# Performance work log

Measured on AMD Instinct MI355X. Metric: run time of the kernel, lower is better.

## Reference

```python
import jax, jax.numpy as jnp
import numpy as np

B, C, W, H = 4, 256, 64, 64
D = C // 8  # reduced query/key channels


def setup_inputs() -> dict:
    key = jax.random.key(0)
    k1, k2, k3, k4, k5 = jax.random.split(key, 5)
    return {
        "x": jax.random.normal(k1, (B, C, W, H), dtype=jnp.float32),
        "q_weight": jax.random.normal(k2, (D, C), dtype=jnp.float32) * 0.05,
        "k_weight": jax.random.normal(k3, (D, C), dtype=jnp.float32) * 0.05,
        "v_weight": jax.random.normal(k4, (C, C), dtype=jnp.float32) * 0.05,
        "gamma": jax.random.normal(k5, (1,), dtype=jnp.float32),
    }


def reference(x, q_weight, k_weight, v_weight, gamma):
    b, c, w, h = x.shape
    n = w * h
    xf = x.reshape(b, c, n)                       # (B, C, N)
    # 1x1 convs == channel matmuls
    q = jnp.einsum('dc,bcn->bdn', q_weight, xf)   # (B, D, N)
    k = jnp.einsum('dc,bcn->bdn', k_weight, xf)   # (B, D, N)
    v = jnp.einsum('oc,bcn->bon', v_weight, xf)   # (B, C, N)
    # energy[b, i, j] = <q[:, i], k[:, j]>  (unscaled, single head)
    energy = jnp.einsum('bdi,bdj->bij', q, k)     # (B, N, N)
    attn = jax.nn.softmax(energy, axis=-1)        # softmax over keys j
    # out[b, c, i] = sum_j v[b, c, j] * attn[b, i, j]
    out = jnp.einsum('bcj,bij->bci', v, attn)     # (B, C, N)
    out = out.reshape(b, c, w, h)
    return gamma[0] * out + x
```

## Files before the change

### kernel.cpp

```cpp
#include <hip/hip_runtime.h>
#include <math.h>

#define Bb 4
#define Cc 256
#define Nn 4096
#define Dd 32
#define CH 128
#define XST 264

typedef __attribute__((ext_vector_type(8))) short bf16x8;
typedef __attribute__((ext_vector_type(4))) float f32x4;

__device__ __forceinline__ unsigned short f2bf(float x) {
    union { float f; unsigned u; } c; c.f = x;
    unsigned r = c.u + 0x7fffu + ((c.u >> 16) & 1u);
    return (unsigned short)(r >> 16);
}
__device__ __forceinline__ unsigned pk2(float a, float b) {
    return (unsigned)f2bf(a) | ((unsigned)f2bf(b) << 16);
}
__device__ __forceinline__ void load_lds16(const void* g, void* l) {
    __builtin_amdgcn_global_load_lds(
        (const __attribute__((address_space(1))) void*)g,
        (__attribute__((address_space(3))) void*)l, 16, 0, 0);
}
__device__ __forceinline__ float fexp2(float x) {
#if __has_builtin(__builtin_amdgcn_exp2f)
    return __builtin_amdgcn_exp2f(x);
#else
    return __exp2f(x);
#endif
}
template <int CTRL>
__device__ __forceinline__ float dppf(float v) {
    int iv = __builtin_bit_cast(int, v);
    return __builtin_bit_cast(float,
        __builtin_amdgcn_update_dpp(iv, iv, CTRL, 0xF, 0xF, false));
}
__device__ __forceinline__ float rowsum16(float v) {
    v += dppf<0xB1>(v);
    v += dppf<0x4E>(v);
    v += dppf<0x141>(v);
    v += dppf<0x140>(v);
    return v;
}

__global__ __launch_bounds__(256) void pack_w(
    const float* __restrict__ qw, const float* __restrict__ kw,
    const float* __restrict__ vw, short* __restrict__ wpk) {
    const int g = blockIdx.x * 256 + threadIdx.x;
    const int qd = g & 3, m = (g >> 2) & 15, kc = (g >> 6) & 7, ot = g >> 9;
    const int o = 16 * ot + m;
    const float* src;
    float scale = 1.0f;
    if (o < 32)      { src = qw + (size_t)o * Cc; scale = 1.44269504088896f; }
    else if (o < 64) { src = kw + (size_t)(o - 32) * Cc; }
    else             { src = vw + (size_t)(o - 64) * Cc; }
    const float* s8 = src + 32 * kc + 8 * qd;
    uint4 u;
    u.x = pk2(s8[0] * scale, s8[1] * scale);
    u.y = pk2(s8[2] * scale, s8[3] * scale);
    u.z = pk2(s8[4] * scale, s8[5] * scale);
    u.w = pk2(s8[6] * scale, s8[7] * scale);
    *(uint4*)(wpk + (size_t)g * 8) = u;
}

__global__ __launch_bounds__(256) void proj(
    const float* __restrict__ x, const short* __restrict__ wpk,
    short* __restrict__ q_t, short* __restrict__ k_t, short* __restrict__ v_b) {
    __shared__ alignas(16) short xs[32 * XST];
    const int b = blockIdx.z;
    const int n0 = blockIdx.x * 32;
    const int tid = threadIdx.x;
    const int w = tid >> 6;
    const int lane = tid & 63, qd = lane >> 4, m = lane & 15;

    {
        const int n = tid & 31, cg = tid >> 5;
        const float* xp = x + ((size_t)b * Cc + 32 * cg) * Nn + n0 + n;
        float xv[32];
#pragma unroll
        for (int i = 0; i < 32; ++i) xv[i] = xp[(size_t)i * Nn];
        short* row = xs + n * XST + 32 * cg;
#pragma unroll
        for (int u4 = 0; u4 < 4; ++u4)
            *(uint4*)(row + 8 * u4) = make_uint4(
                pk2(xv[8*u4+0], xv[8*u4+1]), pk2(xv[8*u4+2], xv[8*u4+3]),
                pk2(xv[8*u4+4], xv[8*u4+5]), pk2(xv[8*u4+6], xv[8*u4+7]));
    }
    __syncthreads();

    const int fslot = m * 4 + qd;
    f32x4 acc[5][2];
#pragma unroll
    for (int i = 0; i < 5; ++i)
#pragma unroll
        for (int nt = 0; nt < 2; ++nt) acc[i][nt] = (f32x4){0.f, 0.f, 0.f, 0.f};

    bf16x8 afc[5], afn[5];
#pragma unroll
    for (int i = 0; i < 5; ++i)
        afc[i] = *(const bf16x8*)(wpk + ((size_t)((4*i + w) * 8 + 0) * 64 + fslot) * 8);

    for (int kc = 0; kc < 8; ++kc) {
        if (kc < 7) {
#pragma unroll
            for (int i = 0; i < 5; ++i)
                afn[i] = *(const bf16x8*)(
                    wpk + ((size_t)((4*i + w) * 8 + kc + 1) * 64 + fslot) * 8);
        }
        const bf16x8 b0 = *(const bf16x8*)&xs[(     m) * XST + 32 * kc + 8 * qd];
        const bf16x8 b1 = *(const bf16x8*)&xs[(16 + m) * XST + 32 * kc + 8 * qd];
#pragma unroll
        for (int i = 0; i < 5; ++i)
            acc[i][0] = __builtin_amdgcn_mfma_f32_16x16x32_bf16(afc[i], b0, acc[i][0], 0, 0, 0);
#pragma unroll
        for (int i = 0; i < 5; ++i)
            acc[i][1] = __builtin_amdgcn_mfma_f32_16x16x32_bf16(afc[i], b1, acc[i][1], 0, 0, 0);
#pragma unroll
        for (int i = 0; i < 5; ++i) afc[i] = afn[i];
    }

#pragma unroll
    for (int i = 0; i < 5; ++i) {
        const int ot = 4 * i + w;
        if (ot < 4) {
            short* dst = (ot < 2 ? q_t : k_t) + (size_t)b * Nn * Dd;
            const int dbase = (ot & 1) * 16 + 4 * qd;
#pragma unroll
            for (int nt = 0; nt < 2; ++nt) {
                const f32x4 a = acc[i][nt];
                *(uint2*)(dst + (size_t)(n0 + 16 * nt + m) * Dd + dbase) =
                    make_uint2(pk2(a[0], a[1]), pk2(a[2], a[3]));
            }
        } else {
            const int cbase = (ot - 4) * 16 + 4 * qd;
            const int gbase = n0 & ~63;
            const int off2 = (n0 & 32) ? 2 : 0;
#pragma unroll
            for (int rr = 0; rr < 4; ++rr) {
                const unsigned pv = pk2(acc[i][0][rr], acc[i][1][rr]);
                *(unsigned*)(v_b + ((size_t)b * Cc + cbase + rr) * Nn +
                             gbase + 4 * m + off2) = pv;
            }
        }
    }
}

__global__ __launch_bounds__(256) void attn(
    const float* __restrict__ x, const short* __restrict__ q_t,
    const short* __restrict__ k_t, const short* __restrict__ v_b,
    const float* __restrict__ gamma, float* __restrict__ out) {
    __shared__ alignas(16) char pool[54528];
    short* q_s = (short*)(pool);
    char*  kv0 = pool + 4096;
    char*  kv1 = pool + 24576;
    short* p_s = (short*)(pool + 45056);
    float* l_s = (float*)(pool + 54272);
    float* o_t = (float*)(pool + 4096);

    const int b = blockIdx.z, cg = blockIdx.y;
    const int i0 = blockIdx.x * 64;
    const int tid = threadIdx.x;
    const int w = tid >> 6, lane = tid & 63;
    const int qd = lane >> 4, m = lane & 15;

    const short* ktb = k_t + (size_t)b * Nn * Dd;
    const short* vtb = v_b + ((size_t)(b * Cc) + cg * CH) * Nn;

    load_lds16(q_t + ((size_t)b * Nn + i0) * Dd + tid * 8, q_s + tid * 8);
    {
        load_lds16(ktb + tid * 8, kv0 + tid * 16);
        short* vls = (short*)(kv0 + 4096);
#pragma unroll
        for (int p = 0; p < 4; ++p) {
            const int cl = 32 * p + (tid >> 3);
            const int j8 = (tid & 7) ^ (cl & 7);
            load_lds16(vtb + (size_t)cl * Nn + j8 * 8, vls + 2048 * p + tid * 8);
        }
    }
    __syncthreads();

    const bf16x8 af = *(const bf16x8*)(q_s + (16 * w + m) * Dd + 8 * qd);

    f32x4 oacc[4][2];
#pragma unroll
    for (int mt = 0; mt < 4; ++mt)
#pragma unroll
        for (int nt = 0; nt < 2; ++nt) oacc[mt][nt] = (f32x4){0.f, 0.f, 0.f, 0.f};
    float l_i[4] = {0.f, 0.f, 0.f, 0.f};

    int cur = 0;
    for (int jt = 0; jt < Nn / 64; ++jt) {
        const char* kvc = cur ? kv1 : kv0;
        const short* k_s = (const short*)kvc;
        const short* v_s = (const short*)(kvc + 4096);

        if (jt) __syncthreads();

        f32x4 sf[4];
#pragma unroll
        for (int nt = 0; nt < 4; ++nt) {
            const bf16x8 bfr = *(const bf16x8*)(k_s + (16 * nt + m) * Dd + 8 * qd);
            sf[nt] = __builtin_amdgcn_mfma_f32_16x16x32_bf16(
                af, bfr, (f32x4){0.f, 0.f, 0.f, 0.f}, 0, 0, 0);
        }

#pragma unroll
        for (int rr = 0; rr < 4; ++rr) {
            float p0 = fexp2(sf[0][rr]);
            float p1 = fexp2(sf[1][rr]);
            float p2 = fexp2(sf[2][rr]);
            float p3 = fexp2(sf[3][rr]);
            l_i[rr] += (p0 + p1) + (p2 + p3);
            *(uint2*)&p_s[(16 * w + 4 * qd + rr) * 72 + 4 * m] =
                make_uint2(pk2(p0, p1), pk2(p2, p3));
        }
        __syncthreads();

        if (jt + 1 < Nn / 64) {
            char* kvn = cur ? kv0 : kv1;
            const int j0n = (jt + 1) * 64;
            load_lds16(ktb + (size_t)j0n * Dd + tid * 8, kvn + tid * 16);
            short* vls = (short*)(kvn + 4096);
#pragma unroll
            for (int p = 0; p < 4; ++p) {
                const int cl = 32 * p + (tid >> 3);
                const int j8 = (tid & 7) ^ (cl & 7);
                load_lds16(vtb + (size_t)cl * Nn + j0n + j8 * 8,
                           vls + 2048 * p + tid * 8);
            }
        }

#pragma unroll
        for (int kc = 0; kc < 2; ++kc) {
            bf16x8 pa[4];
#pragma unroll
            for (int mt = 0; mt < 4; ++mt)
                pa[mt] = *(const bf16x8*)&p_s[(16 * mt + m) * 72 + 32 * kc + 8 * qd];
#pragma unroll
            for (int nt = 0; nt < 2; ++nt) {
                const int cl = 32 * w + 16 * nt + m;
                const bf16x8 vb8 = *(const bf16x8*)(
                    v_s + cl * 64 + (((qd + 4 * kc) ^ (cl & 7)) * 8));
#pragma unroll
                for (int mt = 0; mt < 4; ++mt)
                    oacc[mt][nt] = __builtin_amdgcn_mfma_f32_16x16x32_bf16(
                        pa[mt], vb8, oacc[mt][nt], 0, 0, 0);
            }
        }
        cur ^= 1;
    }

#pragma unroll
    for (int rr = 0; rr < 4; ++rr) l_i[rr] = rowsum16(l_i[rr]);
    if (m == 0)
        *(f32x4*)&l_s[16 * w + 4 * qd] = (f32x4){l_i[0], l_i[1], l_i[2], l_i[3]};

    const float g = gamma[0];
#pragma unroll
    for (int ntp = 0; ntp < 2; ++ntp) {
        __syncthreads();
#pragma unroll
        for (int mt = 0; mt < 4; ++mt)
#pragma unroll
            for (int rr = 0; rr < 4; ++rr)
                o_t[(16 * mt + 4 * qd + rr) * 68 + 16 * w + m] = oacc[mt][ntp][rr];
        __syncthreads();
        const int i = lane;
        const float linv = 1.0f / l_s[i];
#pragma unroll
        for (int kk = 0; kk < 16; ++kk) {
            const int cp = w * 16 + kk;
            const int c = cg * CH + 32 * w + 16 * ntp + kk;
            const float val = o_t[i * 68 + cp] * linv;
            const size_t gidx = ((size_t)b * Cc + c) * Nn + i0 + i;
            out[gidx] = g * val + x[gidx];
        }
    }
}

extern "C" void kernel_launch(void* const* d_in, const int* in_sizes, int n_in,
                              void* d_out, int out_size, void* d_ws, size_t ws_size,
                              hipStream_t stream) {
    const float* x     = (const float*)d_in[0];
    const float* qw    = (const float*)d_in[1];
    const float* kw    = (const float*)d_in[2];
    const float* vw    = (const float*)d_in[3];
    const float* gamma = (const float*)d_in[4];
    float* out = (float*)d_out;

    short* q_t = (short*)d_ws;
    short* k_t = q_t + (size_t)Bb * Nn * Dd;
    short* v_b = k_t + (size_t)Bb * Nn * Dd;
    short* wpk = v_b + (size_t)Bb * Cc * Nn;

    pack_w<<<dim3(40), 256, 0, stream>>>(qw, kw, vw, wpk);
    proj<<<dim3(Nn / 32, 1, Bb), 256, 0, stream>>>(x, wpk, q_t, k_t, v_b);
    attn<<<dim3(Nn / 64, Cc / CH, Bb), 256, 0, stream>>>(x, q_t, k_t, v_b,
                                                         gamma, out);
}
```

Measured before the change: 154.6 us.

## Merge channel groups into one 512-thread block, load V fragments directly from global

The attention kernel now uses a single 512-thread block per 64-query tile covering all 256 channels, instead of two blocks each handling 128 channels. This avoids recomputing QK^T and the exponentials twice per query tile. The score computation is split across two wave groups, each doing half the key columns, and their row sums are combined at the end. V fragments are read straight from global memory into registers rather than staged through LDS, which shrinks LDS use but leaves V reads less coalesced and not prefetched. The grid also halves, which may reduce occupancy and parallelism.

```diff
diff --git a/kernel.cpp b/kernel.cpp
--- a/kernel.cpp
+++ b/kernel.cpp
@@ -5,7 +5,6 @@
 #define Cc 256
 #define Nn 4096
 #define Dd 32
-#define CH 128
 #define XST 264
 
 typedef __attribute__((ext_vector_type(8))) short bf16x8;
@@ -147,90 +146,77 @@
     }
 }
 
-__global__ __launch_bounds__(256) void attn(
+__global__ __launch_bounds__(512) void attn(
     const float* __restrict__ x, const short* __restrict__ q_t,
     const short* __restrict__ k_t, const short* __restrict__ v_b,
     const float* __restrict__ gamma, float* __restrict__ out) {
-    __shared__ alignas(16) char pool[54528];
-    short* q_s = (short*)(pool);
-    char*  kv0 = pool + 4096;
-    char*  kv1 = pool + 24576;
-    short* p_s = (short*)(pool + 45056);
-    float* l_s = (float*)(pool + 54272);
-    float* o_t = (float*)(pool + 4096);
-
-    const int b = blockIdx.z, cg = blockIdx.y;
+    __shared__ alignas(16) char pool[34304];
+    short* q_s = (short*)pool;
+    short* p_s = (short*)(pool + 12288);
+    float* o_t = (float*)pool;
+    float* l_s = (float*)(pool + 33792);
+
+    const int b  = blockIdx.z;
     const int i0 = blockIdx.x * 64;
     const int tid = threadIdx.x;
     const int w = tid >> 6, lane = tid & 63;
     const int qd = lane >> 4, m = lane & 15;
+    const int rt = w & 3, kh = w >> 2;
 
     const short* ktb = k_t + (size_t)b * Nn * Dd;
-    const short* vtb = v_b + ((size_t)(b * Cc) + cg * CH) * Nn;
-
-    load_lds16(q_t + ((size_t)b * Nn + i0) * Dd + tid * 8, q_s + tid * 8);
-    {
-        load_lds16(ktb + tid * 8, kv0 + tid * 16);
-        short* vls = (short*)(kv0 + 4096);
-#pragma unroll
-        for (int p = 0; p < 4; ++p) {
-            const int cl = 32 * p + (tid >> 3);
-            const int j8 = (tid & 7) ^ (cl & 7);
-            load_lds16(vtb + (size_t)cl * Nn + j8 * 8, vls + 2048 * p + tid * 8);
-        }
+    const short* vpb = v_b + ((size_t)(b * Cc) + 32 * w + m) * Nn + 8 * qd;
+
+    if (tid < 256) {
+        load_lds16(q_t + ((size_t)b * Nn + i0) * Dd + tid * 8, q_s + tid * 8);
+    } else {
+        load_lds16(ktb + (size_t)(tid - 256) * 8,
+                   (short*)(pool + 4096) + (tid - 256) * 8);
     }
     __syncthreads();
 
-    const bf16x8 af = *(const bf16x8*)(q_s + (16 * w + m) * Dd + 8 * qd);
+    const bf16x8 af = *(const bf16x8*)(q_s + (16 * rt + m) * Dd + 8 * qd);
 
     f32x4 oacc[4][2];
 #pragma unroll
     for (int mt = 0; mt < 4; ++mt)
 #pragma unroll
-        for (int nt = 0; nt < 2; ++nt) oacc[mt][nt] = (f32x4){0.f, 0.f, 0.f, 0.f};
+        for (int ct = 0; ct < 2; ++ct) oacc[mt][ct] = (f32x4){0.f, 0.f, 0.f, 0.f};
     float l_i[4] = {0.f, 0.f, 0.f, 0.f};
 
     int cur = 0;
     for (int jt = 0; jt < Nn / 64; ++jt) {
-        const char* kvc = cur ? kv1 : kv0;
-        const short* k_s = (const short*)kvc;
-        const short* v_s = (const short*)(kvc + 4096);
-
+        const int j0 = jt * 64;
+        const short* k_s = (const short*)(pool + 4096 + 4096 * cur);
         if (jt) __syncthreads();
 
-        f32x4 sf[4];
-#pragma unroll
-        for (int nt = 0; nt < 4; ++nt) {
-            const bf16x8 bfr = *(const bf16x8*)(k_s + (16 * nt + m) * Dd + 8 * qd);
-            sf[nt] = __builtin_amdgcn_mfma_f32_16x16x32_bf16(
-                af, bfr, (f32x4){0.f, 0.f, 0.f, 0.f}, 0, 0, 0);
-        }
+        bf16x8 vf[2][2];
+#pragma unroll
+        for (int ct = 0; ct < 2; ++ct)
+#pragma unroll
+            for (int kc = 0; kc < 2; ++kc)
+                vf[ct][kc] = *(const bf16x8*)(
+                    vpb + (size_t)(16 * ct) * Nn + j0 + 32 * kc);
+
+        const bf16x8 bk0 = *(const bf16x8*)(k_s + (16 * (2 * kh + 0) + m) * Dd + 8 * qd);
+        const bf16x8 bk1 = *(const bf16x8*)(k_s + (16 * (2 * kh + 1) + m) * Dd + 8 * qd);
+        const f32x4 s0 = __builtin_amdgcn_mfma_f32_16x16x32_bf16(
+            af, bk0, (f32x4){0.f, 0.f, 0.f, 0.f}, 0, 0, 0);
+        const f32x4 s1 = __builtin_amdgcn_mfma_f32_16x16x32_bf16(
+            af, bk1, (f32x4){0.f, 0.f, 0.f, 0.f}, 0, 0, 0);
 
 #pragma unroll
         for (int rr = 0; rr < 4; ++rr) {
-            float p0 = fexp2(sf[0][rr]);
-            float p1 = fexp2(sf[1][rr]);
-            float p2 = fexp2(sf[2][rr]);
-            float p3 = fexp2(sf[3][rr]);
-            l_i[rr] += (p0 + p1) + (p2 + p3);
-            *(uint2*)&p_s[(16 * w + 4 * qd + rr) * 72 + 4 * m] =
-                make_uint2(pk2(p0, p1), pk2(p2, p3));
+            const float p0 = fexp2(s0[rr]);
+            const float p1 = fexp2(s1[rr]);
+            l_i[rr] += p0 + p1;
+            *(unsigned*)&p_s[(16 * rt + 4 * qd + rr) * 72 + 4 * m + 2 * kh] =
+                pk2(p0, p1);
         }
         __syncthreads();
 
-        if (jt + 1 < Nn / 64) {
-            char* kvn = cur ? kv0 : kv1;
-            const int j0n = (jt + 1) * 64;
-            load_lds16(ktb + (size_t)j0n * Dd + tid * 8, kvn + tid * 16);
-            short* vls = (short*)(kvn + 4096);
-#pragma unroll
-            for (int p = 0; p < 4; ++p) {
-                const int cl = 32 * p + (tid >> 3);
-                const int j8 = (tid & 7) ^ (cl & 7);
-                load_lds16(vtb + (size_t)cl * Nn + j0n + j8 * 8,
-                           vls + 2048 * p + tid * 8);
-            }
-        }
+        if (jt + 1 < Nn / 64 && tid >= 256)
+            load_lds16(ktb + (size_t)(j0 + 64) * Dd + (tid - 256) * 8,
+                       (short*)(pool + 4096 + 4096 * (cur ^ 1)) + (tid - 256) * 8);
 
 #pragma unroll
         for (int kc = 0; kc < 2; ++kc) {
@@ -239,15 +225,11 @@
             for (int mt = 0; mt < 4; ++mt)
                 pa[mt] = *(const bf16x8*)&p_s[(16 * mt + m) * 72 + 32 * kc + 8 * qd];
 #pragma unroll
-            for (int nt = 0; nt < 2; ++nt) {
-                const int cl = 32 * w + 16 * nt + m;
-                const bf16x8 vb8 = *(const bf16x8*)(
-                    v_s + cl * 64 + (((qd + 4 * kc) ^ (cl & 7)) * 8));
+            for (int ct = 0; ct < 2; ++ct)
 #pragma unroll
                 for (int mt = 0; mt < 4; ++mt)
-                    oacc[mt][nt] = __builtin_amdgcn_mfma_f32_16x16x32_bf16(
-                        pa[mt], vb8, oacc[mt][nt], 0, 0, 0);
-            }
+                    oacc[mt][ct] = __builtin_amdgcn_mfma_f32_16x16x32_bf16(
+                        pa[mt], vf[ct][kc], oacc[mt][ct], 0, 0, 0);
         }
         cur ^= 1;
     }
@@ -255,27 +237,31 @@
 #pragma unroll
     for (int rr = 0; rr < 4; ++rr) l_i[rr] = rowsum16(l_i[rr]);
     if (m == 0)
-        *(f32x4*)&l_s[16 * w + 4 * qd] = (f32x4){l_i[0], l_i[1], l_i[2], l_i[3]};
+        *(f32x4*)&l_s[kh * 64 + 16 * rt + 4 * qd] =
+            (f32x4){l_i[0], l_i[1], l_i[2], l_i[3]};
+    __syncthreads();
 
     const float g = gamma[0];
-#pragma unroll
-    for (int ntp = 0; ntp < 2; ++ntp) {
+    const int i = lane;
+    const float linv = 1.0f / (l_s[i] + l_s[64 + i]);
+#pragma unroll
+    for (int ps = 0; ps < 2; ++ps) {
+        if (ps) __syncthreads();
+#pragma unroll
+        for (int mt = 0; mt < 4; ++mt)
+#pragma unroll
+            for (int rr = 0; rr < 4; ++rr)
+                o_t[(16 * mt + 4 * qd + rr) * 132 + 16 * w + m] = oacc[mt][ps][rr];
         __syncthreads();
 #pragma unroll
-        for (int mt = 0; mt < 4; ++mt)
-#pragma unroll
-            for (int rr = 0; rr < 4; ++rr)
-                o_t[(16 * mt + 4 * qd + rr) * 68 + 16 * w + m] = oacc[mt][ntp][rr];
-        __syncthreads();
-        const int i = lane;
-        const float linv = 1.0f / l_s[i];
-#pragma unroll
-        for (int kk = 0; kk < 16; ++kk) {
-            const int cp = w * 16 + kk;
-            const int c = cg * CH + 32 * w + 16 * ntp + kk;
-            const float val = o_t[i * 68 + cp] * linv;
-            const size_t gidx = ((size_t)b * Cc + c) * Nn + i0 + i;
-            out[gidx] = g * val + x[gidx];
+        for (int u = 0; u < 4; ++u) {
+            const f32x4 v4 = *(const f32x4*)&o_t[i * 132 + 16 * w + 4 * u];
+#pragma unroll
+            for (int e = 0; e < 4; ++e) {
+                const int c = 32 * w + 16 * ps + 4 * u + e;
+                const size_t gidx = ((size_t)b * Cc + c) * Nn + i0 + i;
+                out[gidx] = g * v4[e] * linv + x[gidx];
+            }
         }
     }
 }
@@ -297,6 +283,5 @@
 
     pack_w<<<dim3(40), 256, 0, stream>>>(qw, kw, vw, wpk);
     proj<<<dim3(Nn / 32, 1, Bb), 256, 0, stream>>>(x, wpk, q_t, k_t, v_b);
-    attn<<<dim3(Nn / 64, Cc / CH, Bb), 256, 0, stream>>>(x, q_t, k_t, v_b,
-                                                         gamma, out);
-}
+    attn<<<dim3(Nn / 64, 1, Bb), 512, 0, stream>>>(x, q_t, k_t, v_b, gamma, out);
+}
```

Result: slower. 175.1 us (+13.3%).
